# Kernel optimization log

Hardware: AMD Instinct MI355X
Metric: run time of the kernel (lower is better)

## Reference

```python
import jax, jax.numpy as jnp
import numpy as np

N, E, F, H, ADD = 50000, 640000, 128, 128, 4
K = N // 2          # SAGPooling ratio=0.5 -> ceil(0.5*N)
EPS = 1e-5          # BatchNorm eps
NEG_SLOPE = 0.2     # GATConv leaky_relu slope


def _prelu(x, a):
    return jnp.where(x >= 0, x, a * x)


def _bn(x, w, b):
    # track_running_stats=False -> always use batch stats (biased var)
    mu = jnp.mean(x, axis=0)
    var = jnp.var(x, axis=0)
    return (x - mu) * jax.lax.rsqrt(var + EPS) * w + b


def _gat(x, src, dst, n, w, a_src, a_dst, bias):
    # GATConv(heads=1, aggr='max', add_self_loops=True)
    loop = jnp.arange(n)
    src = jnp.concatenate([src, loop])
    dst = jnp.concatenate([dst, loop])
    xw = x @ w                                        # [n, H]
    e = jax.nn.leaky_relu((xw @ a_src)[src] + (xw @ a_dst)[dst], NEG_SLOPE)
    m = jax.ops.segment_max(e, dst, num_segments=n)   # stable softmax per dst
    ex = jnp.exp(e - m[dst])
    alpha = ex / jax.ops.segment_sum(ex, dst, num_segments=n)[dst]
    out = jax.ops.segment_max(alpha[:, None] * xw[src], dst, num_segments=n)
    return out + bias                                 # self loops => all finite


def _sage(x, src, dst, n, wl, bl, wr):
    # SAGEConv(aggr='max'): lin_l(max_j x_j) + lin_r(x_i)
    agg = jax.ops.segment_max(x[src], dst, num_segments=n)
    agg = jnp.where(jnp.isfinite(agg), agg, 0.0)      # isolated nodes -> 0
    return agg @ wl + bl + x @ wr


def _sagpool(x, src, dst, n, wrel, brel, wroot):
    # SAGPooling: score = GraphConv(H, 1) (aggr='add'), topk ratio=0.5, tanh gate
    agg = jax.ops.segment_sum(x[src], dst, num_segments=n)
    score = (agg @ wrel + brel + x @ wroot)[:, 0]
    sv, perm = jax.lax.top_k(score, K)
    return x[perm] * jnp.tanh(sv)[:, None]


def _tower(x, ei, p):
    src, dst = ei[0], ei[1]
    n = x.shape[0]
    h = _gat(x, src, dst, n, p['gat_w'], p['gat_att_src'], p['gat_att_dst'], p['gat_bias'])
    h = _prelu(_bn(h, p['bn1_w'], p['bn1_b']), p['prelu1_a'])
    h = _sage(h, src, dst, n, p['sage_wl'], p['sage_bl'], p['sage_wr'])
    h = _prelu(_bn(h, p['bn2_w'], p['bn2_b']), p['prelu2_a'])
    return _sagpool(h, src, dst, n, p['pool_wrel'], p['pool_brel'], p['pool_wroot'])


def setup_inputs() -> dict:
    key = jax.random.key(0)
    ks = jax.random.split(key, 32)
    s = 0.05
    return {
        'Ax': jax.random.normal(ks[0], (N, F), jnp.float32),
        'Gx': jax.random.normal(ks[1], (N, F), jnp.float32),
        'add_features': jax.random.normal(ks[2], (ADD,), jnp.float32),
        'gat_w': jax.random.normal(ks[3], (F, H)) * s,
        'gat_att_src': jax.random.normal(ks[4], (H,)) * s,
        'gat_att_dst': jax.random.normal(ks[5], (H,)) * s,
        'gat_bias': jnp.zeros((H,), jnp.float32),
        'bn1_w': jnp.ones((H,), jnp.float32),
        'bn1_b': jnp.zeros((H,), jnp.float32),
        'prelu1_a': jnp.full((1,), 0.25, jnp.float32),
        'sage_wl': jax.random.normal(ks[6], (H, H)) * s,
        'sage_bl': jnp.zeros((H,), jnp.float32),
        'sage_wr': jax.random.normal(ks[7], (H, H)) * s,
        'bn2_w': jnp.ones((H,), jnp.float32),
        'bn2_b': jnp.zeros((H,), jnp.float32),
        'prelu2_a': jnp.full((1,), 0.25, jnp.float32),
        'pool_wrel': jax.random.normal(ks[8], (H, 1)) * s,
        'pool_brel': jnp.zeros((1,), jnp.float32),
        'pool_wroot': jax.random.normal(ks[9], (H, 1)) * s,
        'fc1_w': jax.random.normal(ks[10], (H + ADD, H)) * s,
        'fc1_b': jnp.zeros((H,), jnp.float32),
        'fc1_prelu_a': jnp.full((1,), 0.25, jnp.float32),
        'fc2_w1': jax.random.normal(ks[11], (H, H)) * s,
        'fc2_b1': jnp.zeros((H,), jnp.float32),
        'fc2_prelu_a': jnp.full((1,), 0.25, jnp.float32),
        'fc2_w2': jax.random.normal(ks[12], (H, 1)) * s,
        'fc2_b2': jnp.zeros((1,), jnp.float32),
        'fc3_w': jax.random.normal(ks[13], (H, 1)) * s,
        'fc3_b': jnp.zeros((1,), jnp.float32),
        'mult_w': jax.random.normal(ks[14], (H, 1)) * s,
        'mult_b': jnp.zeros((1,), jnp.float32),
        'A_edge_index': jax.random.randint(ks[15], (2, E), 0, N, jnp.int32),
        'G_edge_index': jax.random.randint(ks[16], (2, E), 0, N, jnp.int32),
    }


def reference(Ax, Gx, add_features, gat_w, gat_att_src, gat_att_dst, gat_bias,
              bn1_w, bn1_b, prelu1_a, sage_wl, sage_bl, sage_wr,
              bn2_w, bn2_b, prelu2_a, pool_wrel, pool_brel, pool_wroot,
              fc1_w, fc1_b, fc1_prelu_a, fc2_w1, fc2_b1, fc2_prelu_a,
              fc2_w2, fc2_b2, fc3_w, fc3_b, mult_w, mult_b,
              A_edge_index, G_edge_index):
    p = dict(gat_w=gat_w, gat_att_src=gat_att_src, gat_att_dst=gat_att_dst,
             gat_bias=gat_bias, bn1_w=bn1_w, bn1_b=bn1_b, prelu1_a=prelu1_a,
             sage_wl=sage_wl, sage_bl=sage_bl, sage_wr=sage_wr,
             bn2_w=bn2_w, bn2_b=bn2_b, prelu2_a=prelu2_a,
             pool_wrel=pool_wrel, pool_brel=pool_brel, pool_wroot=pool_wroot)
    Ap = _tower(Ax, A_edge_index, p)              # [K, H]
    Gp = _tower(Gx, G_edge_index, p)              # [K, H]
    ag = jnp.max(jnp.concatenate([Ap, Gp], axis=0), axis=0)   # [H]
    pool = jnp.concatenate([ag, add_features])                # [H+ADD]
    x = _prelu(pool @ fc1_w + fc1_b, fc1_prelu_a)
    x_IV = jnp.exp(_prelu(x @ fc2_w1 + fc2_b1, fc2_prelu_a) @ fc2_w2 + fc2_b2)
    x_Tg = jnp.exp(x @ fc3_w + fc3_b) * jnp.tanh(x @ mult_w + mult_b)
    return x_IV, x_Tg
```

## Files before the change

### kernel.cpp

```cpp
#include <hip/hip_runtime.h>
#include <math.h>

#define NN 50000
#define EE 640000
#define HH 128
#define KK 25000
#define NEG_SLOPE 0.2f
#define TIE_CAP 4096
#define BN_BLOCKS 200

__device__ __forceinline__ float lrelu(float x) { return x >= 0.f ? x : NEG_SLOPE * x; }
__device__ __forceinline__ float prelu(float x, float a) { return x >= 0.f ? x : a * x; }
__device__ __forceinline__ unsigned ford(float f) {
    unsigned u = __float_as_uint(f);
    return (u & 0x80000000u) ? ~u : (u | 0x80000000u);
}
__device__ __forceinline__ float unford(unsigned u) {
    return __uint_as_float((u & 0x80000000u) ? (u & 0x7fffffffu) : ~u);
}

__global__ __launch_bounds__(256) void deg_hist(const int* __restrict__ dst, int* __restrict__ deg) {
    int i = blockIdx.x * 256 + threadIdx.x;
    if (i < EE) atomicAdd(&deg[dst[i]], 1);
}

__global__ __launch_bounds__(1024) void scan_ptr(const int* __restrict__ deg, int* __restrict__ ptr,
                                                 int* __restrict__ cur) {
    __shared__ int csum[1024];
    int c = threadIdx.x;
    int b0 = c * 49, b1 = b0 + 49;
    if (b1 > NN) b1 = NN;
    int s = 0;
    for (int i = b0; i < b1; ++i) s += deg[i];
    csum[c] = s;
    __syncthreads();
    if (c == 0) {
        int acc = 0;
        for (int i = 0; i < 1024; ++i) { int t = csum[i]; csum[i] = acc; acc += t; }
        ptr[NN] = acc;
    }
    __syncthreads();
    int acc = csum[c];
    for (int i = b0; i < b1; ++i) { ptr[i] = acc; cur[i] = acc; acc += deg[i]; }
}

__global__ __launch_bounds__(256) void scatter_csr(const int* __restrict__ src, const int* __restrict__ dst,
                                                   int* __restrict__ cur, int* __restrict__ csr) {
    int i = blockIdx.x * 256 + threadIdx.x;
    if (i < EE) {
        int p = atomicAdd(&cur[dst[i]], 1);
        csr[p] = src[i];
    }
}

__global__ __launch_bounds__(256) void gemm128(const float* __restrict__ A, const float* __restrict__ W,
                                               const float* __restrict__ bias, float* __restrict__ C,
                                               int n, int accflag, int biasflag) {
    __shared__ float sW[128 * 128];
    __shared__ float sA[32 * 132];
    for (int i = threadIdx.x; i < 4096; i += 256)
        ((float4*)sW)[i] = ((const float4*)W)[i];
    int row0 = blockIdx.x * 32;
    int nrows = n - row0; if (nrows > 32) nrows = 32;
    for (int i = threadIdx.x; i < 1024; i += 256) {
        int r = i >> 5, c4 = i & 31;
        if (r < nrows)
            *((float4*)(sA + r * 132 + c4 * 4)) = ((const float4*)(A + (size_t)(row0 + r) * 128))[c4];
    }
    __syncthreads();
    int tr = threadIdx.x >> 4;
    int c0 = (threadIdx.x & 15) * 4;
    float a00[4] = {0,0,0,0}, a01[4] = {0,0,0,0}, a10[4] = {0,0,0,0}, a11[4] = {0,0,0,0};
    const float* a0p = sA + (tr * 2) * 132;
    const float* a1p = a0p + 132;
    for (int k = 0; k < 128; ++k) {
        float a0 = a0p[k], a1 = a1p[k];
        float4 w0 = *(const float4*)(sW + k * 128 + c0);
        float4 w1 = *(const float4*)(sW + k * 128 + c0 + 64);
        a00[0] = fmaf(a0, w0.x, a00[0]); a00[1] = fmaf(a0, w0.y, a00[1]);
        a00[2] = fmaf(a0, w0.z, a00[2]); a00[3] = fmaf(a0, w0.w, a00[3]);
        a01[0] = fmaf(a0, w1.x, a01[0]); a01[1] = fmaf(a0, w1.y, a01[1]);
        a01[2] = fmaf(a0, w1.z, a01[2]); a01[3] = fmaf(a0, w1.w, a01[3]);
        a10[0] = fmaf(a1, w0.x, a10[0]); a10[1] = fmaf(a1, w0.y, a10[1]);
        a10[2] = fmaf(a1, w0.z, a10[2]); a10[3] = fmaf(a1, w0.w, a10[3]);
        a11[0] = fmaf(a1, w1.x, a11[0]); a11[1] = fmaf(a1, w1.y, a11[1]);
        a11[2] = fmaf(a1, w1.z, a11[2]); a11[3] = fmaf(a1, w1.w, a11[3]);
    }
    float b0[4] = {0,0,0,0}, b1[4] = {0,0,0,0};
    if (biasflag) {
        #pragma unroll
        for (int u = 0; u < 4; ++u) { b0[u] = bias[c0 + u]; b1[u] = bias[c0 + 64 + u]; }
    }
    #pragma unroll
    for (int rr = 0; rr < 2; ++rr) {
        int r = row0 + tr * 2 + rr;
        if (r < n) {
            float* op = C + (size_t)r * 128;
            float vlo[4], vhi[4];
            #pragma unroll
            for (int u = 0; u < 4; ++u) {
                vlo[u] = (rr ? a10[u] : a00[u]) + b0[u];
                vhi[u] = (rr ? a11[u] : a01[u]) + b1[u];
            }
            if (accflag) {
                float4 o0 = *(float4*)(op + c0);
                float4 o1 = *(float4*)(op + c0 + 64);
                vlo[0] += o0.x; vlo[1] += o0.y; vlo[2] += o0.z; vlo[3] += o0.w;
                vhi[0] += o1.x; vhi[1] += o1.y; vhi[2] += o1.z; vhi[3] += o1.w;
            }
            *(float4*)(op + c0)      = make_float4(vlo[0], vlo[1], vlo[2], vlo[3]);
            *(float4*)(op + c0 + 64) = make_float4(vhi[0], vhi[1], vhi[2], vhi[3]);
        }
    }
}

__global__ __launch_bounds__(256) void att_scores(const float* __restrict__ xw, const float* __restrict__ asrc,
                                                  const float* __restrict__ adst, float* __restrict__ ssrc,
                                                  float* __restrict__ sdst) {
    int wid = (blockIdx.x * 256 + threadIdx.x) >> 6;
    int lane = threadIdx.x & 63;
    if (wid >= NN) return;
    float x0 = xw[(size_t)wid * 128 + lane];
    float x1 = xw[(size_t)wid * 128 + lane + 64];
    float ps = x0 * asrc[lane] + x1 * asrc[lane + 64];
    float pd = x0 * adst[lane] + x1 * adst[lane + 64];
    #pragma unroll
    for (int o = 32; o; o >>= 1) { ps += __shfl_xor(ps, o); pd += __shfl_xor(pd, o); }
    if (lane == 0) { ssrc[wid] = ps; sdst[wid] = pd; }
}

__global__ __launch_bounds__(256) void gat_agg(const float* __restrict__ xw, const int* __restrict__ csr,
                                               const int* __restrict__ ptr, const float* __restrict__ ssrc,
                                               const float* __restrict__ sdst, const float* __restrict__ bias,
                                               float* __restrict__ ealpha, float* __restrict__ out) {
    int wid = (blockIdx.x * 256 + threadIdx.x) >> 6;
    int lane = threadIdx.x & 63;
    if (wid >= NN) return;
    int s = ptr[wid], e = ptr[wid + 1];
    float sd = sdst[wid];
    float selfval = lrelu(ssrc[wid] + sd);
    float m = selfval;
    for (int i = s + lane; i < e; i += 64) m = fmaxf(m, lrelu(ssrc[csr[i]] + sd));
    #pragma unroll
    for (int o = 32; o; o >>= 1) m = fmaxf(m, __shfl_xor(m, o));
    float sum = (lane == 0) ? __expf(selfval - m) : 0.f;
    for (int i = s + lane; i < e; i += 64) {
        float ex = __expf(lrelu(ssrc[csr[i]] + sd) - m);
        ealpha[i] = ex;
        sum += ex;
    }
    #pragma unroll
    for (int o = 32; o; o >>= 1) sum += __shfl_xor(sum, o);
    float inv = 1.f / sum;
    float aself = __expf(selfval - m) * inv;
    float f0 = aself * xw[(size_t)wid * 128 + lane];
    float f1 = aself * xw[(size_t)wid * 128 + lane + 64];
    int i = s;
    for (; i + 4 <= e; i += 4) {
        int s0 = csr[i], s1 = csr[i + 1], s2 = csr[i + 2], s3 = csr[i + 3];
        float al0 = ealpha[i] * inv, al1 = ealpha[i + 1] * inv;
        float al2 = ealpha[i + 2] * inv, al3 = ealpha[i + 3] * inv;
        const float* p0 = xw + (size_t)s0 * 128;
        const float* p1 = xw + (size_t)s1 * 128;
        const float* p2 = xw + (size_t)s2 * 128;
        const float* p3 = xw + (size_t)s3 * 128;
        float x00 = p0[lane], x01 = p0[lane + 64];
        float x10 = p1[lane], x11 = p1[lane + 64];
        float x20 = p2[lane], x21 = p2[lane + 64];
        float x30 = p3[lane], x31 = p3[lane + 64];
        f0 = fmaxf(fmaxf(fmaxf(fmaxf(f0, al0 * x00), al1 * x10), al2 * x20), al3 * x30);
        f1 = fmaxf(fmaxf(fmaxf(fmaxf(f1, al0 * x01), al1 * x11), al2 * x21), al3 * x31);
    }
    for (; i < e; ++i) {
        int src = csr[i];
        float a = ealpha[i] * inv;
        f0 = fmaxf(f0, a * xw[(size_t)src * 128 + lane]);
        f1 = fmaxf(f1, a * xw[(size_t)src * 128 + lane + 64]);
    }
    out[(size_t)wid * 128 + lane] = f0 + bias[lane];
    out[(size_t)wid * 128 + lane + 64] = f1 + bias[lane + 64];
}

__global__ __launch_bounds__(256) void bn_stage1(const float* __restrict__ x, float* __restrict__ psum,
                                                 float* __restrict__ psq) {
    int col = threadIdx.x & 127, sub = threadIdx.x >> 7;
    int r0 = blockIdx.x * 250, r1 = r0 + 250;
    float s = 0.f, q = 0.f;
    for (int r = r0 + sub; r < r1; r += 2) {
        float v = x[(size_t)r * 128 + col];
        s += v;
        q = fmaf(v, v, q);
    }
    __shared__ float ls[256], lq[256];
    ls[threadIdx.x] = s; lq[threadIdx.x] = q;
    __syncthreads();
    if (sub == 0) {
        psum[blockIdx.x * 128 + col] = ls[col] + ls[col + 128];
        psq[blockIdx.x * 128 + col] = lq[col] + lq[col + 128];
    }
}

__global__ __launch_bounds__(128) void bn_stage2(const float* __restrict__ psum, const float* __restrict__ psq,
                                                 const float* __restrict__ w, const float* __restrict__ b,
                                                 float* __restrict__ scale, float* __restrict__ shift) {
    int c = threadIdx.x;
    double s = 0.0, q = 0.0;
    for (int i = 0; i < BN_BLOCKS; ++i) { s += (double)psum[i * 128 + c]; q += (double)psq[i * 128 + c]; }
    double mu = s / NN;
    double var = q / NN - mu * mu;
    if (var < 0.0) var = 0.0;
    float rs = (float)(1.0 / sqrt(var + 1e-5));
    float sc = rs * w[c];
    scale[c] = sc;
    shift[c] = b[c] - (float)mu * sc;
}

__global__ __launch_bounds__(256) void bn_prelu_apply(float* __restrict__ x, const float* __restrict__ scale,
                                                      const float* __restrict__ shift, const float* __restrict__ pa) {
    int i = blockIdx.x * 256 + threadIdx.x;
    float a = pa[0];
    float4 v = ((float4*)x)[i];
    int c = (i * 4) & 127;
    v.x = v.x * scale[c]     + shift[c];     v.x = prelu(v.x, a);
    v.y = v.y * scale[c + 1] + shift[c + 1]; v.y = prelu(v.y, a);
    v.z = v.z * scale[c + 2] + shift[c + 2]; v.z = prelu(v.z, a);
    v.w = v.w * scale[c + 3] + shift[c + 3]; v.w = prelu(v.w, a);
    ((float4*)x)[i] = v;
}

__global__ __launch_bounds__(256) void max_agg(const float* __restrict__ h1, const int* __restrict__ csr,
                                               const int* __restrict__ ptr, float* __restrict__ agg) {
    int wid = (blockIdx.x * 256 + threadIdx.x) >> 6;
    int lane = threadIdx.x & 63;
    if (wid >= NN) return;
    int s = ptr[wid], e = ptr[wid + 1];
    float m0 = -INFINITY, m1 = -INFINITY;
    int i = s;
    for (; i + 4 <= e; i += 4) {
        int s0 = csr[i], s1 = csr[i + 1], s2 = csr[i + 2], s3 = csr[i + 3];
        const float* p0 = h1 + (size_t)s0 * 128;
        const float* p1 = h1 + (size_t)s1 * 128;
        const float* p2 = h1 + (size_t)s2 * 128;
        const float* p3 = h1 + (size_t)s3 * 128;
        float x00 = p0[lane], x01 = p0[lane + 64];
        float x10 = p1[lane], x11 = p1[lane + 64];
        float x20 = p2[lane], x21 = p2[lane + 64];
        float x30 = p3[lane], x31 = p3[lane + 64];
        m0 = fmaxf(fmaxf(fmaxf(fmaxf(m0, x00), x10), x20), x30);
        m1 = fmaxf(fmaxf(fmaxf(fmaxf(m1, x01), x11), x21), x31);
    }
    for (; i < e; ++i) {
        int src = csr[i];
        m0 = fmaxf(m0, h1[(size_t)src * 128 + lane]);
        m1 = fmaxf(m1, h1[(size_t)src * 128 + lane + 64]);
    }
    if (s == e) { m0 = 0.f; m1 = 0.f; }
    agg[(size_t)wid * 128 + lane] = m0;
    agg[(size_t)wid * 128 + lane + 64] = m1;
}

__global__ __launch_bounds__(256) void node_dots(const float* __restrict__ h2, const float* __restrict__ wrel,
                                                 const float* __restrict__ wroot, float* __restrict__ pr,
                                                 float* __restrict__ rootdot) {
    int wid = (blockIdx.x * 256 + threadIdx.x) >> 6;
    int lane = threadIdx.x & 63;
    if (wid >= NN) return;
    float x0 = h2[(size_t)wid * 128 + lane];
    float x1 = h2[(size_t)wid * 128 + lane + 64];
    float p = x0 * wrel[lane] + x1 * wrel[lane + 64];
    float r = x0 * wroot[lane] + x1 * wroot[lane + 64];
    #pragma unroll
    for (int o = 32; o; o >>= 1) { p += __shfl_xor(p, o); r += __shfl_xor(r, o); }
    if (lane == 0) { pr[wid] = p; rootdot[wid] = r; }
}

__global__ __launch_bounds__(256) void score_k(const float* __restrict__ pr, const float* __restrict__ rootdot,
                                               const int* __restrict__ csr, const int* __restrict__ ptr,
                                               const float* __restrict__ brel, float* __restrict__ score,
                                               unsigned* __restrict__ su) {
    int d = blockIdx.x * 256 + threadIdx.x;
    if (d >= NN) return;
    int s = ptr[d], e = ptr[d + 1];
    float acc = 0.f;
    for (int i = s; i < e; ++i) acc += pr[csr[i]];
    float sc = acc + rootdot[d] + brel[0];
    score[d] = sc;
    su[d] = ford(sc);
}

__global__ __launch_bounds__(256) void hist_hi_k(const unsigned* __restrict__ su, unsigned* __restrict__ hist) {
    int i = blockIdx.x * 256 + threadIdx.x;
    if (i < NN) atomicAdd(&hist[su[i] >> 16], 1u);
}

__global__ __launch_bounds__(1024) void scan_hi(const unsigned* __restrict__ hist, unsigned* __restrict__ selst) {
    __shared__ unsigned csum[1024];
    int c = threadIdx.x;
    unsigned s = 0;
    const unsigned* hp = hist + c * 64;
    for (int j = 0; j < 64; ++j) s += hp[j];
    csum[c] = s;
    __syncthreads();
    if (c == 0) {
        unsigned cum = 0;
        int chunk = 1023;
        for (; chunk > 0; --chunk) { if (cum + csum[chunk] >= KK) break; cum += csum[chunk]; }
        int b = chunk * 64 + 63;
        for (; b > chunk * 64; --b) { if (cum + hist[b] >= KK) break; cum += hist[b]; }
        selst[0] = (unsigned)b;
        selst[1] = cum;
    }
}

__global__ __launch_bounds__(256) void hist_lo_k(const unsigned* __restrict__ su, const unsigned* __restrict__ selst,
                                                 unsigned* __restrict__ histlo) {
    int i = blockIdx.x * 256 + threadIdx.x;
    if (i < NN) {
        unsigned u = su[i];
        if ((u >> 16) == selst[0]) atomicAdd(&histlo[u & 0xffffu], 1u);
    }
}

__global__ __launch_bounds__(1024) void scan_lo(const unsigned* __restrict__ histlo, unsigned* __restrict__ selst) {
    __shared__ unsigned csum[1024];
    int c = threadIdx.x;
    unsigned s = 0;
    const unsigned* hp = histlo + c * 64;
    for (int j = 0; j < 64; ++j) s += hp[j];
    csum[c] = s;
    __syncthreads();
    if (c == 0) {
        unsigned cum = selst[1];
        int chunk = 1023;
        for (; chunk > 0; --chunk) { if (cum + csum[chunk] >= KK) break; cum += csum[chunk]; }
        int b = chunk * 64 + 63;
        for (; b > chunk * 64; --b) { if (cum + histlo[b] >= KK) break; cum += histlo[b]; }
        unsigned tu = (selst[0] << 16) | (unsigned)b;
        selst[2] = tu;
        selst[3] = KK - cum;
    }
}

__global__ __launch_bounds__(256) void select_colmax(const float* __restrict__ h2, const float* __restrict__ score,
                                                     const unsigned* __restrict__ su, const unsigned* __restrict__ selst,
                                                     unsigned* __restrict__ ties, unsigned* __restrict__ tiecnt,
                                                     unsigned* __restrict__ colmax) {
    unsigned tu = selst[2];
    int col = threadIdx.x & 127, sub = threadIdx.x >> 7;
    int r0 = blockIdx.x * 250, r1 = r0 + 250;
    float m = -INFINITY;
    for (int r = r0 + sub; r < r1; r += 2) {
        unsigned u = su[r];
        if (u > tu) {
            float g = tanhf(score[r]);
            m = fmaxf(m, g * h2[(size_t)r * 128 + col]);
        } else if (u == tu && col == 0) {
            unsigned p = atomicAdd(tiecnt, 1u);
            if (p < TIE_CAP) ties[p] = (unsigned)r;
        }
    }
    __shared__ float ls[256];
    ls[threadIdx.x] = m;
    __syncthreads();
    if (sub == 0) {
        float mm = fmaxf(ls[col], ls[col + 128]);
        if (mm > -INFINITY) atomicMax(&colmax[col], ford(mm));
    }
}

__global__ __launch_bounds__(128) void tie_resolve(const float* __restrict__ h2, const float* __restrict__ score,
                                                   const unsigned* __restrict__ selst, const unsigned* __restrict__ ties,
                                                   unsigned* __restrict__ colmax) {
    __shared__ unsigned chosen;
    int R = (int)selst[3];
    int tc = (int)selst[4];
    if (tc > TIE_CAP) tc = TIE_CAP;
    int t = threadIdx.x;
    unsigned last = 0;
    int iters = R < tc ? R : tc;
    for (int it = 0; it < iters; ++it) {
        if (t == 0) {
            unsigned best = 0xffffffffu;
            for (int j = 0; j < tc; ++j) {
                unsigned v = ties[j];
                if (v >= last && v < best) best = v;
            }
            chosen = best;
        }
        __syncthreads();
        unsigned row = chosen;
        if (row != 0xffffffffu) {
            float g = tanhf(score[row]);
            atomicMax(&colmax[t], ford(g * h2[(size_t)row * 128 + t]));
        }
        __syncthreads();
        if (t == 0) last = chosen + 1;
    }
}

__global__ __launch_bounds__(128) void head_k(const unsigned* __restrict__ colmax, const float* __restrict__ addf,
                                              const float* __restrict__ fc1w, const float* __restrict__ fc1b,
                                              const float* __restrict__ fa1, const float* __restrict__ w21,
                                              const float* __restrict__ b21, const float* __restrict__ fa2,
                                              const float* __restrict__ w22, const float* __restrict__ b22,
                                              const float* __restrict__ w3, const float* __restrict__ b3,
                                              const float* __restrict__ wm, const float* __restrict__ bm,
                                              float* __restrict__ out) {
    __shared__ float ag[132], xv[128], yv[128], red0[128], red1[128], red2[128];
    int t = threadIdx.x;
    ag[t] = fmaxf(unford(colmax[t]), unford(colmax[128 + t]));
    if (t < 4) ag[128 + t] = addf[t];
    __syncthreads();
    float s = fc1b[t];
    for (int k = 0; k < 132; ++k) s = fmaf(ag[k], fc1w[k * 128 + t], s);
    xv[t] = prelu(s, fa1[0]);
    __syncthreads();
    float s2 = b21[t];
    for (int k = 0; k < 128; ++k) s2 = fmaf(xv[k], w21[k * 128 + t], s2);
    yv[t] = prelu(s2, fa2[0]);
    __syncthreads();
    red0[t] = yv[t] * w22[t];
    red1[t] = xv[t] * w3[t];
    red2[t] = xv[t] * wm[t];
    __syncthreads();
    if (t == 0) {
        float r0 = 0.f, r1 = 0.f, r2 = 0.f;
        for (int k = 0; k < 128; ++k) { r0 += red0[k]; r1 += red1[k]; r2 += red2[k]; }
        out[0] = expf(r0 + b22[0]);
        out[1] = expf(r1 + b3[0]) * tanhf(r2 + bm[0]);
    }
}

extern "C" void kernel_launch(void* const* d_in, const int* in_sizes, int n_in,
                              void* d_out, int out_size, void* d_ws, size_t ws_size,
                              hipStream_t stream) {
    const float* Ax    = (const float*)d_in[0];
    const float* Gx    = (const float*)d_in[1];
    const float* addf  = (const float*)d_in[2];
    const float* gatw  = (const float*)d_in[3];
    const float* asrc  = (const float*)d_in[4];
    const float* adst  = (const float*)d_in[5];
    const float* gbias = (const float*)d_in[6];
    const float* bn1w  = (const float*)d_in[7];
    const float* bn1b  = (const float*)d_in[8];
    const float* pa1   = (const float*)d_in[9];
    const float* wl    = (const float*)d_in[10];
    const float* bl    = (const float*)d_in[11];
    const float* wr    = (const float*)d_in[12];
    const float* bn2w  = (const float*)d_in[13];
    const float* bn2b  = (const float*)d_in[14];
    const float* pa2   = (const float*)d_in[15];
    const float* wrel  = (const float*)d_in[16];
    const float* brel  = (const float*)d_in[17];
    const float* wroot = (const float*)d_in[18];
    const float* fc1w  = (const float*)d_in[19];
    const float* fc1b  = (const float*)d_in[20];
    const float* fa1   = (const float*)d_in[21];
    const float* w21   = (const float*)d_in[22];
    const float* b21   = (const float*)d_in[23];
    const float* fa2   = (const float*)d_in[24];
    const float* w22   = (const float*)d_in[25];
    const float* b22   = (const float*)d_in[26];
    const float* w3    = (const float*)d_in[27];
    const float* b3    = (const float*)d_in[28];
    const float* wm    = (const float*)d_in[29];
    const float* bm    = (const float*)d_in[30];
    const int*   Aei   = (const int*)d_in[31];
    const int*   Gei   = (const int*)d_in[32];
    float* out = (float*)d_out;

    char* wp = (char*)d_ws;
    auto alloc = [&](size_t bytes) -> char* {
        char* p = wp;
        wp += (bytes + 255) & ~(size_t)255;
        return p;
    };
    float*    big1   = (float*)alloc((size_t)NN * HH * 4);
    float*    big2   = (float*)alloc((size_t)NN * HH * 4);
    int*      csr    = (int*)alloc((size_t)EE * 4);
    float*    ealpha = (float*)alloc((size_t)EE * 4);
    int*      ptr    = (int*)alloc((NN + 1) * 4);
    int*      cur    = (int*)alloc(NN * 4);
    int*      deg    = (int*)alloc(NN * 4);
    float*    ssrc   = (float*)alloc(NN * 4);
    float*    sdst   = (float*)alloc(NN * 4);
    float*    score  = (float*)alloc(NN * 4);
    unsigned* su     = (unsigned*)alloc(NN * 4);
    float*    psum   = (float*)alloc(BN_BLOCKS * 128 * 4);
    float*    psq    = (float*)alloc(BN_BLOCKS * 128 * 4);
    float*    scale  = (float*)alloc(128 * 4);
    float*    shift  = (float*)alloc(128 * 4);
    unsigned* hist   = (unsigned*)alloc(65536 * 4);
    unsigned* histlo = (unsigned*)alloc(65536 * 4);
    unsigned* selst  = (unsigned*)alloc(8 * 4);
    unsigned* ties   = (unsigned*)alloc(TIE_CAP * 4);
    unsigned* colmax = (unsigned*)alloc(2 * 128 * 4);

    hipMemsetAsync(colmax, 0, 2 * 128 * 4, stream);

    for (int t = 0; t < 2; ++t) {
        const float* x   = (t == 0) ? Ax : Gx;
        const int* ei    = (t == 0) ? Aei : Gei;
        const int* esrc  = ei;
        const int* edst  = ei + EE;

        hipMemsetAsync(deg, 0, NN * 4, stream);
        hipMemsetAsync(hist, 0, 65536 * 4, stream);
        hipMemsetAsync(histlo, 0, 65536 * 4, stream);
        hipMemsetAsync(selst, 0, 8 * 4, stream);

        deg_hist<<<EE / 256, 256, 0, stream>>>(edst, deg);
        scan_ptr<<<1, 1024, 0, stream>>>(deg, ptr, cur);
        scatter_csr<<<EE / 256, 256, 0, stream>>>(esrc, edst, cur, csr);

        gemm128<<<(NN + 31) / 32, 256, 0, stream>>>(x, gatw, nullptr, big1, NN, 0, 0);
        att_scores<<<(NN + 3) / 4, 256, 0, stream>>>(big1, asrc, adst, ssrc, sdst);
        gat_agg<<<(NN + 3) / 4, 256, 0, stream>>>(big1, csr, ptr, ssrc, sdst, gbias, ealpha, big2);
        bn_stage1<<<BN_BLOCKS, 256, 0, stream>>>(big2, psum, psq);
        bn_stage2<<<1, 128, 0, stream>>>(psum, psq, bn1w, bn1b, scale, shift);
        bn_prelu_apply<<<NN * 128 / 4 / 256, 256, 0, stream>>>(big2, scale, shift, pa1);

        max_agg<<<(NN + 3) / 4, 256, 0, stream>>>(big2, csr, ptr, big1);
        gemm128<<<(NN + 31) / 32, 256, 0, stream>>>(big1, wl, bl, big1, NN, 0, 1);
        gemm128<<<(NN + 31) / 32, 256, 0, stream>>>(big2, wr, nullptr, big1, NN, 1, 0);
        bn_stage1<<<BN_BLOCKS, 256, 0, stream>>>(big1, psum, psq);
        bn_stage2<<<1, 128, 0, stream>>>(psum, psq, bn2w, bn2b, scale, shift);
        bn_prelu_apply<<<NN * 128 / 4 / 256, 256, 0, stream>>>(big1, scale, shift, pa2);

        node_dots<<<(NN + 3) / 4, 256, 0, stream>>>(big1, wrel, wroot, ssrc, sdst);
        score_k<<<(NN + 255) / 256, 256, 0, stream>>>(ssrc, sdst, csr, ptr, brel, score, su);
        hist_hi_k<<<(NN + 255) / 256, 256, 0, stream>>>(su, hist);
        scan_hi<<<1, 1024, 0, stream>>>(hist, selst);
        hist_lo_k<<<(NN + 255) / 256, 256, 0, stream>>>(su, selst, histlo);
        scan_lo<<<1, 1024, 0, stream>>>(histlo, selst);
        select_colmax<<<200, 256, 0, stream>>>(big1, score, su, selst, ties, selst + 4, colmax + t * 128);
        tie_resolve<<<1, 128, 0, stream>>>(big1, score, selst, ties, colmax + t * 128);
    }

    head_k<<<1, 128, 0, stream>>>(colmax, addf, fc1w, fc1b, fa1, w21, b21, fa2,
                                  w22, b22, w3, b3, wm, bm, out);
}
```

Baseline: 1.635 ms.

## Parallelize CSR scan, fuse attention and pooling dots, online softmax, smaller GEMM smem

Replaces the single-block serial prefix scan with a three-stage multi-block scan. Fuses the GAT attention-score dots into the GEMM epilogue, the BN/PReLU apply with the pooling node dots, and the top-k histogram into score computation. GAT aggregation now uses a single-pass online softmax that stores logits and recomputes the exponentials in the gather loop. The GEMM stages weights in four 32-row k-tiles, cutting shared memory for more occupancy at the cost of extra barriers, and the separate memsets are merged into one call that assumes contiguous workspace buffers.

```diff
diff --git a/kernel.cpp b/kernel.cpp
--- a/kernel.cpp
+++ b/kernel.cpp
@@ -8,6 +8,7 @@
 #define NEG_SLOPE 0.2f
 #define TIE_CAP 4096
 #define BN_BLOCKS 200
+#define NSB 98
 
 __device__ __forceinline__ float lrelu(float x) { return x >= 0.f ? x : NEG_SLOPE * x; }
 __device__ __forceinline__ float prelu(float x, float a) { return x >= 0.f ? x : a * x; }
@@ -24,24 +25,47 @@
     if (i < EE) atomicAdd(&deg[dst[i]], 1);
 }
 
-__global__ __launch_bounds__(1024) void scan_ptr(const int* __restrict__ deg, int* __restrict__ ptr,
-                                                 int* __restrict__ cur) {
-    __shared__ int csum[1024];
-    int c = threadIdx.x;
-    int b0 = c * 49, b1 = b0 + 49;
-    if (b1 > NN) b1 = NN;
-    int s = 0;
-    for (int i = b0; i < b1; ++i) s += deg[i];
-    csum[c] = s;
-    __syncthreads();
-    if (c == 0) {
-        int acc = 0;
-        for (int i = 0; i < 1024; ++i) { int t = csum[i]; csum[i] = acc; acc += t; }
-        ptr[NN] = acc;
-    }
-    __syncthreads();
-    int acc = csum[c];
-    for (int i = b0; i < b1; ++i) { ptr[i] = acc; cur[i] = acc; acc += deg[i]; }
+__global__ __launch_bounds__(512) void scan_s1(const int* __restrict__ deg, int* __restrict__ ptr,
+                                               int* __restrict__ bsum) {
+    __shared__ int tmp[512];
+    int g = blockIdx.x * 512 + threadIdx.x;
+    int v = (g < NN) ? deg[g] : 0;
+    tmp[threadIdx.x] = v;
+    __syncthreads();
+    for (int o = 1; o < 512; o <<= 1) {
+        int add = (threadIdx.x >= o) ? tmp[threadIdx.x - o] : 0;
+        __syncthreads();
+        tmp[threadIdx.x] += add;
+        __syncthreads();
+    }
+    if (g < NN) ptr[g] = tmp[threadIdx.x] - v;
+    if (threadIdx.x == 511) bsum[blockIdx.x] = tmp[511];
+}
+
+__global__ __launch_bounds__(128) void scan_s2(int* __restrict__ bsum, int* __restrict__ ptr) {
+    __shared__ int tmp[128];
+    int t = threadIdx.x;
+    int v = (t < NSB) ? bsum[t] : 0;
+    tmp[t] = v;
+    __syncthreads();
+    for (int o = 1; o < 128; o <<= 1) {
+        int add = (t >= o) ? tmp[t - o] : 0;
+        __syncthreads();
+        tmp[t] += add;
+        __syncthreads();
+    }
+    if (t < NSB) bsum[t] = tmp[t] - v;
+    if (t == 127) ptr[NN] = tmp[127];
+}
+
+__global__ __launch_bounds__(512) void scan_s3(int* __restrict__ ptr, const int* __restrict__ bsum,
+                                               int* __restrict__ cur) {
+    int g = blockIdx.x * 512 + threadIdx.x;
+    if (g < NN) {
+        int v = ptr[g] + bsum[blockIdx.x];
+        ptr[g] = v;
+        cur[g] = v;
+    }
 }
 
 __global__ __launch_bounds__(256) void scatter_csr(const int* __restrict__ src, const int* __restrict__ dst,
@@ -55,11 +79,11 @@
 
 __global__ __launch_bounds__(256) void gemm128(const float* __restrict__ A, const float* __restrict__ W,
                                                const float* __restrict__ bias, float* __restrict__ C,
-                                               int n, int accflag, int biasflag) {
-    __shared__ float sW[128 * 128];
+                                               int n, int accflag, int biasflag,
+                                               const float* __restrict__ asrc, const float* __restrict__ adst,
+                                               float* __restrict__ ssrc_o, float* __restrict__ sdst_o) {
+    __shared__ float sW[32 * 128];
     __shared__ float sA[32 * 132];
-    for (int i = threadIdx.x; i < 4096; i += 256)
-        ((float4*)sW)[i] = ((const float4*)W)[i];
     int row0 = blockIdx.x * 32;
     int nrows = n - row0; if (nrows > 32) nrows = 32;
     for (int i = threadIdx.x; i < 1024; i += 256) {
@@ -67,24 +91,30 @@
         if (r < nrows)
             *((float4*)(sA + r * 132 + c4 * 4)) = ((const float4*)(A + (size_t)(row0 + r) * 128))[c4];
     }
-    __syncthreads();
     int tr = threadIdx.x >> 4;
     int c0 = (threadIdx.x & 15) * 4;
     float a00[4] = {0,0,0,0}, a01[4] = {0,0,0,0}, a10[4] = {0,0,0,0}, a11[4] = {0,0,0,0};
     const float* a0p = sA + (tr * 2) * 132;
     const float* a1p = a0p + 132;
-    for (int k = 0; k < 128; ++k) {
-        float a0 = a0p[k], a1 = a1p[k];
-        float4 w0 = *(const float4*)(sW + k * 128 + c0);
-        float4 w1 = *(const float4*)(sW + k * 128 + c0 + 64);
-        a00[0] = fmaf(a0, w0.x, a00[0]); a00[1] = fmaf(a0, w0.y, a00[1]);
-        a00[2] = fmaf(a0, w0.z, a00[2]); a00[3] = fmaf(a0, w0.w, a00[3]);
-        a01[0] = fmaf(a0, w1.x, a01[0]); a01[1] = fmaf(a0, w1.y, a01[1]);
-        a01[2] = fmaf(a0, w1.z, a01[2]); a01[3] = fmaf(a0, w1.w, a01[3]);
-        a10[0] = fmaf(a1, w0.x, a10[0]); a10[1] = fmaf(a1, w0.y, a10[1]);
-        a10[2] = fmaf(a1, w0.z, a10[2]); a10[3] = fmaf(a1, w0.w, a10[3]);
-        a11[0] = fmaf(a1, w1.x, a11[0]); a11[1] = fmaf(a1, w1.y, a11[1]);
-        a11[2] = fmaf(a1, w1.z, a11[2]); a11[3] = fmaf(a1, w1.w, a11[3]);
+    for (int kt = 0; kt < 4; ++kt) {
+        __syncthreads();
+        for (int i = threadIdx.x; i < 1024; i += 256)
+            ((float4*)sW)[i] = ((const float4*)W)[kt * 1024 + i];
+        __syncthreads();
+        int kb = kt * 32;
+        for (int k = 0; k < 32; ++k) {
+            float a0 = a0p[kb + k], a1 = a1p[kb + k];
+            float4 w0 = *(const float4*)(sW + k * 128 + c0);
+            float4 w1 = *(const float4*)(sW + k * 128 + c0 + 64);
+            a00[0] = fmaf(a0, w0.x, a00[0]); a00[1] = fmaf(a0, w0.y, a00[1]);
+            a00[2] = fmaf(a0, w0.z, a00[2]); a00[3] = fmaf(a0, w0.w, a00[3]);
+            a01[0] = fmaf(a0, w1.x, a01[0]); a01[1] = fmaf(a0, w1.y, a01[1]);
+            a01[2] = fmaf(a0, w1.z, a01[2]); a01[3] = fmaf(a0, w1.w, a01[3]);
+            a10[0] = fmaf(a1, w0.x, a10[0]); a10[1] = fmaf(a1, w0.y, a10[1]);
+            a10[2] = fmaf(a1, w0.z, a10[2]); a10[3] = fmaf(a1, w0.w, a10[3]);
+            a11[0] = fmaf(a1, w1.x, a11[0]); a11[1] = fmaf(a1, w1.y, a11[1]);
+            a11[2] = fmaf(a1, w1.z, a11[2]); a11[3] = fmaf(a1, w1.w, a11[3]);
+        }
     }
     float b0[4] = {0,0,0,0}, b1[4] = {0,0,0,0};
     if (biasflag) {
@@ -112,21 +142,28 @@
             *(float4*)(op + c0 + 64) = make_float4(vhi[0], vhi[1], vhi[2], vhi[3]);
         }
     }
-}
-
-__global__ __launch_bounds__(256) void att_scores(const float* __restrict__ xw, const float* __restrict__ asrc,
-                                                  const float* __restrict__ adst, float* __restrict__ ssrc,
-                                                  float* __restrict__ sdst) {
-    int wid = (blockIdx.x * 256 + threadIdx.x) >> 6;
-    int lane = threadIdx.x & 63;
-    if (wid >= NN) return;
-    float x0 = xw[(size_t)wid * 128 + lane];
-    float x1 = xw[(size_t)wid * 128 + lane + 64];
-    float ps = x0 * asrc[lane] + x1 * asrc[lane + 64];
-    float pd = x0 * adst[lane] + x1 * adst[lane + 64];
-    #pragma unroll
-    for (int o = 32; o; o >>= 1) { ps += __shfl_xor(ps, o); pd += __shfl_xor(pd, o); }
-    if (lane == 0) { ssrc[wid] = ps; sdst[wid] = pd; }
+    if (ssrc_o) {
+        float ps0 = 0.f, pd0 = 0.f, ps1 = 0.f, pd1 = 0.f;
+        #pragma unroll
+        for (int u = 0; u < 4; ++u) {
+            float w0s = asrc[c0 + u], w1s = asrc[c0 + 64 + u];
+            float w0d = adst[c0 + u], w1d = adst[c0 + 64 + u];
+            ps0 += a00[u] * w0s + a01[u] * w1s;
+            pd0 += a00[u] * w0d + a01[u] * w1d;
+            ps1 += a10[u] * w0s + a11[u] * w1s;
+            pd1 += a10[u] * w0d + a11[u] * w1d;
+        }
+        #pragma unroll
+        for (int o = 1; o < 16; o <<= 1) {
+            ps0 += __shfl_xor(ps0, o); pd0 += __shfl_xor(pd0, o);
+            ps1 += __shfl_xor(ps1, o); pd1 += __shfl_xor(pd1, o);
+        }
+        if ((threadIdx.x & 15) == 0) {
+            int r = row0 + tr * 2;
+            if (r < n)     { ssrc_o[r] = ps0;     sdst_o[r] = pd0; }
+            if (r + 1 < n) { ssrc_o[r + 1] = ps1; sdst_o[r + 1] = pd1; }
+        }
+    }
 }
 
 __global__ __launch_bounds__(256) void gat_agg(const float* __restrict__ xw, const int* __restrict__ csr,
@@ -139,27 +176,33 @@
     int s = ptr[wid], e = ptr[wid + 1];
     float sd = sdst[wid];
     float selfval = lrelu(ssrc[wid] + sd);
-    float m = selfval;
-    for (int i = s + lane; i < e; i += 64) m = fmaxf(m, lrelu(ssrc[csr[i]] + sd));
+    float m = -1e30f, sum = 0.f;
+    if (lane == 0) { m = selfval; sum = 1.f; }
+    for (int i = s + lane; i < e; i += 64) {
+        float v = lrelu(ssrc[csr[i]] + sd);
+        ealpha[i] = v;
+        float nm = fmaxf(m, v);
+        sum = sum * __expf(m - nm) + __expf(v - nm);
+        m = nm;
+    }
     #pragma unroll
-    for (int o = 32; o; o >>= 1) m = fmaxf(m, __shfl_xor(m, o));
-    float sum = (lane == 0) ? __expf(selfval - m) : 0.f;
-    for (int i = s + lane; i < e; i += 64) {
-        float ex = __expf(lrelu(ssrc[csr[i]] + sd) - m);
-        ealpha[i] = ex;
-        sum += ex;
-    }
-    #pragma unroll
-    for (int o = 32; o; o >>= 1) sum += __shfl_xor(sum, o);
+    for (int o = 1; o < 64; o <<= 1) {
+        float om = __shfl_xor(m, o);
+        float os = __shfl_xor(sum, o);
+        float nm = fmaxf(m, om);
+        sum = sum * __expf(m - nm) + os * __expf(om - nm);
+        m = nm;
+    }
     float inv = 1.f / sum;
+    asm volatile("s_waitcnt vmcnt(0)" ::: "memory");
     float aself = __expf(selfval - m) * inv;
     float f0 = aself * xw[(size_t)wid * 128 + lane];
     float f1 = aself * xw[(size_t)wid * 128 + lane + 64];
     int i = s;
     for (; i + 4 <= e; i += 4) {
         int s0 = csr[i], s1 = csr[i + 1], s2 = csr[i + 2], s3 = csr[i + 3];
-        float al0 = ealpha[i] * inv, al1 = ealpha[i + 1] * inv;
-        float al2 = ealpha[i + 2] * inv, al3 = ealpha[i + 3] * inv;
+        float al0 = __expf(ealpha[i] - m) * inv,     al1 = __expf(ealpha[i + 1] - m) * inv;
+        float al2 = __expf(ealpha[i + 2] - m) * inv, al3 = __expf(ealpha[i + 3] - m) * inv;
         const float* p0 = xw + (size_t)s0 * 128;
         const float* p1 = xw + (size_t)s1 * 128;
         const float* p2 = xw + (size_t)s2 * 128;
@@ -173,7 +216,7 @@
     }
     for (; i < e; ++i) {
         int src = csr[i];
-        float a = ealpha[i] * inv;
+        float a = __expf(ealpha[i] - m) * inv;
         f0 = fmaxf(f0, a * xw[(size_t)src * 128 + lane]);
         f1 = fmaxf(f1, a * xw[(size_t)src * 128 + lane + 64]);
     }
@@ -226,6 +269,30 @@
     v.z = v.z * scale[c + 2] + shift[c + 2]; v.z = prelu(v.z, a);
     v.w = v.w * scale[c + 3] + shift[c + 3]; v.w = prelu(v.w, a);
     ((float4*)x)[i] = v;
+}
+
+__global__ __launch_bounds__(256) void bn_prelu_dots(float* __restrict__ x, const float* __restrict__ scale,
+                                                     const float* __restrict__ shift, const float* __restrict__ pa,
+                                                     const float* __restrict__ wrel, const float* __restrict__ wroot,
+                                                     float* __restrict__ pr, float* __restrict__ rootdot) {
+    int gw = (blockIdx.x * 256 + threadIdx.x) >> 6;
+    int lane = threadIdx.x & 63;
+    if (gw >= NN / 2) return;
+    int row = gw * 2 + (lane >> 5);
+    int cq = lane & 31;
+    int c = cq * 4;
+    float a = pa[0];
+    float4 v = ((float4*)x)[(size_t)row * 32 + cq];
+    v.x = prelu(v.x * scale[c]     + shift[c],     a);
+    v.y = prelu(v.y * scale[c + 1] + shift[c + 1], a);
+    v.z = prelu(v.z * scale[c + 2] + shift[c + 2], a);
+    v.w = prelu(v.w * scale[c + 3] + shift[c + 3], a);
+    ((float4*)x)[(size_t)row * 32 + cq] = v;
+    float p = v.x * wrel[c] + v.y * wrel[c + 1] + v.z * wrel[c + 2] + v.w * wrel[c + 3];
+    float r = v.x * wroot[c] + v.y * wroot[c + 1] + v.z * wroot[c + 2] + v.w * wroot[c + 3];
+    #pragma unroll
+    for (int o = 1; o < 32; o <<= 1) { p += __shfl_xor(p, o); r += __shfl_xor(r, o); }
+    if (cq == 0) { pr[row] = p; rootdot[row] = r; }
 }
 
 __global__ __launch_bounds__(256) void max_agg(const float* __restrict__ h1, const int* __restrict__ csr,
@@ -259,25 +326,10 @@
     agg[(size_t)wid * 128 + lane + 64] = m1;
 }
 
-__global__ __launch_bounds__(256) void node_dots(const float* __restrict__ h2, const float* __restrict__ wrel,
-                                                 const float* __restrict__ wroot, float* __restrict__ pr,
-                                                 float* __restrict__ rootdot) {
-    int wid = (blockIdx.x * 256 + threadIdx.x) >> 6;
-    int lane = threadIdx.x & 63;
-    if (wid >= NN) return;
-    float x0 = h2[(size_t)wid * 128 + lane];
-    float x1 = h2[(size_t)wid * 128 + lane + 64];
-    float p = x0 * wrel[lane] + x1 * wrel[lane + 64];
-    float r = x0 * wroot[lane] + x1 * wroot[lane + 64];
-    #pragma unroll
-    for (int o = 32; o; o >>= 1) { p += __shfl_xor(p, o); r += __shfl_xor(r, o); }
-    if (lane == 0) { pr[wid] = p; rootdot[wid] = r; }
-}
-
 __global__ __launch_bounds__(256) void score_k(const float* __restrict__ pr, const float* __restrict__ rootdot,
                                                const int* __restrict__ csr, const int* __restrict__ ptr,
                                                const float* __restrict__ brel, float* __restrict__ score,
-                                               unsigned* __restrict__ su) {
+                                               unsigned* __restrict__ su, unsigned* __restrict__ hist) {
     int d = blockIdx.x * 256 + threadIdx.x;
     if (d >= NN) return;
     int s = ptr[d], e = ptr[d + 1];
@@ -285,12 +337,9 @@
     for (int i = s; i < e; ++i) acc += pr[csr[i]];
     float sc = acc + rootdot[d] + brel[0];
     score[d] = sc;
-    su[d] = ford(sc);
-}
-
-__global__ __launch_bounds__(256) void hist_hi_k(const unsigned* __restrict__ su, unsigned* __restrict__ hist) {
-    int i = blockIdx.x * 256 + threadIdx.x;
-    if (i < NN) atomicAdd(&hist[su[i] >> 16], 1u);
+    unsigned u = ford(sc);
+    su[d] = u;
+    atomicAdd(&hist[u >> 16], 1u);
 }
 
 __global__ __launch_bounds__(1024) void scan_hi(const unsigned* __restrict__ hist, unsigned* __restrict__ selst) {
@@ -482,6 +531,7 @@
     int*      ptr    = (int*)alloc((NN + 1) * 4);
     int*      cur    = (int*)alloc(NN * 4);
     int*      deg    = (int*)alloc(NN * 4);
+    int*      bsum   = (int*)alloc(NSB * 4);
     float*    ssrc   = (float*)alloc(NN * 4);
     float*    sdst   = (float*)alloc(NN * 4);
     float*    score  = (float*)alloc(NN * 4);
@@ -505,31 +555,32 @@
         const int* edst  = ei + EE;
 
         hipMemsetAsync(deg, 0, NN * 4, stream);
-        hipMemsetAsync(hist, 0, 65536 * 4, stream);
-        hipMemsetAsync(histlo, 0, 65536 * 4, stream);
-        hipMemsetAsync(selst, 0, 8 * 4, stream);
+        hipMemsetAsync(hist, 0, 2 * 65536 * 4 + 256, stream);
 
         deg_hist<<<EE / 256, 256, 0, stream>>>(edst, deg);
-        scan_ptr<<<1, 1024, 0, stream>>>(deg, ptr, cur);
+        scan_s1<<<NSB, 512, 0, stream>>>(deg, ptr, bsum);
+        scan_s2<<<1, 128, 0, stream>>>(bsum, ptr);
+        scan_s3<<<NSB, 512, 0, stream>>>(ptr, bsum, cur);
         scatter_csr<<<EE / 256, 256, 0, stream>>>(esrc, edst, cur, csr);
 
-        gemm128<<<(NN + 31) / 32, 256, 0, stream>>>(x, gatw, nullptr, big1, NN, 0, 0);
-        att_scores<<<(NN + 3) / 4, 256, 0, stream>>>(big1, asrc, adst, ssrc, sdst);
+        gemm128<<<(NN + 31) / 32, 256, 0, stream>>>(x, gatw, nullptr, big1, NN, 0, 0,
+                                                    asrc, adst, ssrc, sdst);
         gat_agg<<<(NN + 3) / 4, 256, 0, stream>>>(big1, csr, ptr, ssrc, sdst, gbias, ealpha, big2);
         bn_stage1<<<BN_BLOCKS, 256, 0, stream>>>(big2, psum, psq);
         bn_stage2<<<1, 128, 0, stream>>>(psum, psq, bn1w, bn1b, scale, shift);
         bn_prelu_apply<<<NN * 128 / 4 / 256, 256, 0, stream>>>(big2, scale, shift, pa1);
 
         max_agg<<<(NN + 3) / 4, 256, 0, stream>>>(big2, csr, ptr, big1);
-        gemm128<<<(NN + 31) / 32, 256, 0, stream>>>(big1, wl, bl, big1, NN, 0, 1);
-        gemm128<<<(NN + 31) / 32, 256, 0, stream>>>(big2, wr, nullptr, big1, NN, 1, 0);
+        gemm128<<<(NN + 31) / 32, 256, 0, stream>>>(big1, wl, bl, big1, NN, 0, 1,
+                                                    nullptr, nullptr, nullptr, nullptr);
+        gemm128<<<(NN + 31) / 32, 256, 0, stream>>>(big2, wr, nullptr, big1, NN, 1, 0,
+                                                    nullptr, nullptr, nullptr, nullptr);
         bn_stage1<<<BN_BLOCKS, 256, 0, stream>>>(big1, psum, psq);
         bn_stage2<<<1, 128, 0, stream>>>(psum, psq, bn2w, bn2b, scale, shift);
-        bn_prelu_apply<<<NN * 128 / 4 / 256, 256, 0, stream>>>(big1, scale, shift, pa2);
-
-        node_dots<<<(NN + 3) / 4, 256, 0, stream>>>(big1, wrel, wroot, ssrc, sdst);
-        score_k<<<(NN + 255) / 256, 256, 0, stream>>>(ssrc, sdst, csr, ptr, brel, score, su);
-        hist_hi_k<<<(NN + 255) / 256, 256, 0, stream>>>(su, hist);
+        bn_prelu_dots<<<(NN / 2 + 3) / 4, 256, 0, stream>>>(big1, scale, shift, pa2,
+                                                            wrel, wroot, ssrc, sdst);
+
+        score_k<<<(NN + 255) / 256, 256, 0, stream>>>(ssrc, sdst, csr, ptr, brel, score, su, hist);
         scan_hi<<<1, 1024, 0, stream>>>(hist, selst);
         hist_lo_k<<<(NN + 255) / 256, 256, 0, stream>>>(su, selst, histlo);
         scan_lo<<<1, 1024, 0, stream>>>(histlo, selst);
```

Result: faster. 1.368 ms (-16.4%).
